# Performance work log

Hardware: AMD Instinct MI355X
Metric: run time of the kernel (lower is better)

## Reference

```python
import jax, jax.numpy as jnp
import numpy as np

N_NODES = 50000
N_EDGES = 800000
IN_FEATS, N_HIDDEN, OUT_FEATS = 512, 512, 256


def setup_inputs() -> dict:
    key = jax.random.key(0)
    ks = jax.random.split(key, 10)
    features = jax.random.normal(ks[0], (N_NODES, IN_FEATS), dtype=jnp.float32)
    src = jax.random.randint(ks[1], (N_EDGES,), 0, N_NODES, dtype=jnp.int64)
    dst = jax.random.randint(ks[2], (N_EDGES,), 0, N_NODES, dtype=jnp.int64)
    def glorot(k, fan_in, fan_out):
        s = jnp.sqrt(6.0 / (fan_in + fan_out)).astype(jnp.float32)
        return jax.random.uniform(k, (fan_in, fan_out), jnp.float32, -s, s)
    W0 = glorot(ks[3], IN_FEATS, N_HIDDEN)
    b0 = jnp.zeros((N_HIDDEN,), jnp.float32)
    W1 = glorot(ks[4], N_HIDDEN, N_HIDDEN)
    b1 = jnp.zeros((N_HIDDEN,), jnp.float32)
    W2 = glorot(ks[5], N_HIDDEN, OUT_FEATS)
    b2 = jnp.zeros((OUT_FEATS,), jnp.float32)
    return {"features": features, "src": src, "dst": dst,
            "W0": W0, "b0": b0, "W1": W1, "b1": b1, "W2": W2, "b2": b2}


def _graph_conv(x, W, b, src, dst, out_norm, in_norm, activation):
    # DGL GraphConv, norm='both': D_out^{-1/2} A^T D_in^{-1/2}? -> per-node scale,
    # gather on src, segment-sum on dst, scale, linear, bias, activation.
    h = x @ W                               # [N, out] dense GEMM (weight applied first)
    h = h * out_norm[:, None]               # src-side degree norm
    msgs = h[src]                           # [E, out] gather
    agg = jax.ops.segment_sum(msgs, dst, num_segments=x.shape[0])  # [N, out]
    agg = agg * in_norm[:, None] + b
    return activation(agg) if activation is not None else agg


def reference(features, src, dst, W0, b0, W1, b1, W2, b2):
    n = features.shape[0]
    ones = jnp.ones((src.shape[0],), jnp.float32)
    out_deg = jnp.clip(jax.ops.segment_sum(ones, src, num_segments=n), 1.0)
    in_deg = jnp.clip(jax.ops.segment_sum(ones, dst, num_segments=n), 1.0)
    out_norm = jax.lax.rsqrt(out_deg)
    in_norm = jax.lax.rsqrt(in_deg)
    # eval mode: dropout between layers is identity
    h = _graph_conv(features, W0, b0, src, dst, out_norm, in_norm, jax.nn.relu)
    h = _graph_conv(h, W1, b1, src, dst, out_norm, in_norm, jax.nn.relu)
    h = _graph_conv(h, W2, b2, src, dst, out_norm, in_norm, None)
    return h
```

## Files before the change

kernel.cpp:

```cpp
#include <hip/hip_runtime.h>

#define N_NODES 50000
#define N_EDGES 800000

typedef __attribute__((ext_vector_type(8))) _Float16 half8;
typedef __attribute__((ext_vector_type(4))) float f32x4;
typedef __attribute__((ext_vector_type(8))) unsigned short ushort8;

static __device__ __forceinline__ unsigned short f2h(float f) {
    _Float16 h = (_Float16)f;
    return __builtin_bit_cast(unsigned short, h);
}
static __device__ __forceinline__ float h2f(unsigned short u) {
    return (float)__builtin_bit_cast(_Float16, u);
}

static __device__ __forceinline__ void async16(unsigned short* lds, const unsigned short* g) {
    __builtin_amdgcn_global_load_lds(
        (const __attribute__((address_space(1))) void*)g,
        (__attribute__((address_space(3))) void*)lds, 16, 0, 0);
}

__global__ void hist_kernel(const int* __restrict__ src, const int* __restrict__ dst,
                            int* __restrict__ outc, int* __restrict__ inc) {
    int i = blockIdx.x * blockDim.x + threadIdx.x;
    if (i < N_EDGES) {
        atomicAdd(&outc[src[i]], 1);
        atomicAdd(&inc[dst[i]], 1);
    }
}

__global__ void norm_kernel(const int* __restrict__ outc, const int* __restrict__ inc,
                            float* __restrict__ outn, float* __restrict__ inn) {
    int i = blockIdx.x * blockDim.x + threadIdx.x;
    if (i < N_NODES) {
        outn[i] = rsqrtf(fmaxf((float)outc[i], 1.0f));
        inn[i]  = rsqrtf(fmaxf((float)inc[i], 1.0f));
    }
}

__global__ __launch_bounds__(256) void scan1(const int* __restrict__ cnt,
                                             int* __restrict__ row_start,
                                             int* __restrict__ bsum, int n) {
    __shared__ int t[256];
    int tid = threadIdx.x;
    int i = blockIdx.x * 256 + tid;
    int v = (i < n) ? cnt[i] : 0;
    t[tid] = v;
    __syncthreads();
#pragma unroll
    for (int off = 1; off < 256; off <<= 1) {
        int x = (tid >= off) ? t[tid - off] : 0;
        __syncthreads();
        t[tid] += x;
        __syncthreads();
    }
    if (i < n) row_start[i] = t[tid] - v;
    if (tid == 255) bsum[blockIdx.x] = t[255];
}

__global__ __launch_bounds__(256) void scan2(int* __restrict__ bsum,
                                             int* __restrict__ boff,
                                             int* __restrict__ row_start, int nb) {
    __shared__ int t[256];
    int tid = threadIdx.x;
    int v = (tid < nb) ? bsum[tid] : 0;
    t[tid] = v;
    __syncthreads();
#pragma unroll
    for (int off = 1; off < 256; off <<= 1) {
        int x = (tid >= off) ? t[tid - off] : 0;
        __syncthreads();
        t[tid] += x;
        __syncthreads();
    }
    if (tid < nb) boff[tid] = t[tid] - v;
    if (tid == 0) row_start[N_NODES] = N_EDGES;
}

__global__ __launch_bounds__(256) void scan3(int* __restrict__ row_start,
                                             const int* __restrict__ boff, int n) {
    int i = blockIdx.x * 256 + threadIdx.x;
    if (i < n) row_start[i] += boff[blockIdx.x];
}

__global__ void fill_kernel(const int* __restrict__ src, const int* __restrict__ dst,
                            const int* __restrict__ row_start, int* __restrict__ cursor,
                            int* __restrict__ csr_src) {
    int e = blockIdx.x * blockDim.x + threadIdx.x;
    if (e < N_EDGES) {
        int d = dst[e];
        int pos = atomicAdd(&cursor[d], 1);
        csr_src[row_start[d] + pos] = src[e];
    }
}

__global__ __launch_bounds__(256) void conv_W(const float* __restrict__ W,
                                              unsigned short* __restrict__ Wt,
                                              int K, int N) {
    __shared__ float t[32][33];
    int tx = threadIdx.x & 31, ty = threadIdx.x >> 5;
    int kb = blockIdx.x * 32, nb = blockIdx.y * 32;
#pragma unroll
    for (int i = 0; i < 4; ++i)
        t[ty + 8 * i][tx] = W[(size_t)(kb + ty + 8 * i) * N + nb + tx];
    __syncthreads();
#pragma unroll
    for (int i = 0; i < 4; ++i) {
        float v = t[tx][ty + 8 * i];
        int n = nb + ty + 8 * i, k = kb + tx;
        Wt[(size_t)n * K + k] = f2h(v);
    }
}

__global__ void conv_A(const float4* __restrict__ feat4, const float* __restrict__ outn,
                       ushort4* __restrict__ Af, long total4) {
    long i = (long)blockIdx.x * blockDim.x + threadIdx.x;
    if (i >= total4) return;
    int row = (int)(i >> 7);
    float s = outn[row];
    float4 v = feat4[i];
    ushort4 h;
    h.x = f2h(v.x * s);
    h.y = f2h(v.y * s);
    h.z = f2h(v.z * s);
    h.w = f2h(v.w * s);
    Af[i] = h;
}

__global__ __launch_bounds__(256) void gemm_mfma(
    const unsigned short* __restrict__ A, const unsigned short* __restrict__ B,
    unsigned short* __restrict__ C, int M, int N)
{
    const int K = 512;
    __shared__ unsigned short sA[128 * 32];
    __shared__ unsigned short sB[128 * 32];

    const int tid = threadIdx.x;
    const int rowBase = blockIdx.x * 128;
    const int colBase = blockIdx.y * 128;
    const int wave = tid >> 6;
    const int lane = tid & 63;
    const int wr = (wave >> 1) * 64;
    const int wc = (wave & 1) * 64;
    const int lrow = lane & 15;
    const int quad = lane >> 4;

    f32x4 acc[4][4] = {};

    const int crow = tid >> 2;
    const int ck   = (tid & 3) * 8;
    const int ar0 = min(rowBase + crow, M - 1);
    const int ar1 = min(rowBase + 64 + crow, M - 1);
    const int bn0 = colBase + crow;
    const int bn1 = colBase + 64 + crow;
    const int ldsOf0 = tid * 8;
    const int ldsOf1 = 64 * 32 + tid * 8;

    for (int k0 = 0; k0 < K; k0 += 32) {
        __syncthreads();
        async16(sA + ldsOf0, A + (size_t)ar0 * K + k0 + ck);
        async16(sA + ldsOf1, A + (size_t)ar1 * K + k0 + ck);
        async16(sB + ldsOf0, B + (size_t)bn0 * K + k0 + ck);
        async16(sB + ldsOf1, B + (size_t)bn1 * K + k0 + ck);
        __syncthreads();

        half8 av[4], bv[4];
#pragma unroll
        for (int mt = 0; mt < 4; ++mt)
            av[mt] = *(const half8*)&sA[(wr + mt * 16 + lrow) * 32 + quad * 8];
#pragma unroll
        for (int nt = 0; nt < 4; ++nt)
            bv[nt] = *(const half8*)&sB[(wc + nt * 16 + lrow) * 32 + quad * 8];
#pragma unroll
        for (int mt = 0; mt < 4; ++mt)
#pragma unroll
            for (int nt = 0; nt < 4; ++nt)
                acc[mt][nt] = __builtin_amdgcn_mfma_f32_16x16x32_f16(av[mt], bv[nt], acc[mt][nt], 0, 0, 0);
    }

#pragma unroll
    for (int mt = 0; mt < 4; ++mt) {
        int grow0 = rowBase + wr + mt * 16 + quad * 4;
#pragma unroll
        for (int nt = 0; nt < 4; ++nt) {
            int gcol = colBase + wc + nt * 16 + lrow;
#pragma unroll
            for (int r = 0; r < 4; ++r) {
                int grow = grow0 + r;
                if (grow < M) C[(size_t)grow * N + gcol] = f2h(acc[mt][nt][r]);
            }
        }
    }
}

__global__ __launch_bounds__(64) void agg_f16_512(
    const unsigned short* __restrict__ H, const int* __restrict__ csr_src,
    const int* __restrict__ row_start, const float* __restrict__ inn,
    const float* __restrict__ outn, const float* __restrict__ bias,
    ushort8* __restrict__ Af)
{
    const int d = blockIdx.x;
    const int tid = threadIdx.x;
    const int start = row_start[d];
    const int end   = row_start[d + 1];
    const unsigned short* Hb = H + tid * 8;

    float acc[8] = {};
    int j = start;
    for (; j + 4 <= end; j += 4) {
        int i0 = csr_src[j + 0], i1 = csr_src[j + 1];
        int i2 = csr_src[j + 2], i3 = csr_src[j + 3];
        ushort8 u0 = *(const ushort8*)(Hb + (size_t)i0 * 512);
        ushort8 u1 = *(const ushort8*)(Hb + (size_t)i1 * 512);
        ushort8 u2 = *(const ushort8*)(Hb + (size_t)i2 * 512);
        ushort8 u3 = *(const ushort8*)(Hb + (size_t)i3 * 512);
#pragma unroll
        for (int q = 0; q < 8; ++q) {
            acc[q] += h2f(u0[q]);
            acc[q] += h2f(u1[q]);
            acc[q] += h2f(u2[q]);
            acc[q] += h2f(u3[q]);
        }
    }
    for (; j < end; ++j) {
        int i0 = csr_src[j];
        ushort8 u0 = *(const ushort8*)(Hb + (size_t)i0 * 512);
#pragma unroll
        for (int q = 0; q < 8; ++q) acc[q] += h2f(u0[q]);
    }

    float s = inn[d];
    float so = outn[d];
    float b[8];
    *(float4*)&b[0] = ((const float4*)bias)[tid * 2 + 0];
    *(float4*)&b[4] = ((const float4*)bias)[tid * 2 + 1];
    ushort8 h;
#pragma unroll
    for (int q = 0; q < 8; ++q)
        h[q] = f2h(fmaxf(acc[q] * s + b[q], 0.f) * so);
    Af[(size_t)d * 64 + tid] = h;
}

__global__ __launch_bounds__(64) void agg_f32_256(
    const unsigned short* __restrict__ H, const int* __restrict__ csr_src,
    const int* __restrict__ row_start, const float* __restrict__ inn,
    const float* __restrict__ bias, float4* __restrict__ out)
{
    const int d = blockIdx.x;
    const int tid = threadIdx.x;
    const int start = row_start[d];
    const int end   = row_start[d + 1];
    const unsigned short* Hb = H + tid * 4;

    float acc[4] = {};
    int j = start;
    for (; j + 4 <= end; j += 4) {
        int i0 = csr_src[j + 0], i1 = csr_src[j + 1];
        int i2 = csr_src[j + 2], i3 = csr_src[j + 3];
        ushort4 u0 = *(const ushort4*)(Hb + (size_t)i0 * 256);
        ushort4 u1 = *(const ushort4*)(Hb + (size_t)i1 * 256);
        ushort4 u2 = *(const ushort4*)(Hb + (size_t)i2 * 256);
        ushort4 u3 = *(const ushort4*)(Hb + (size_t)i3 * 256);
        acc[0] += h2f(u0.x) + h2f(u1.x) + h2f(u2.x) + h2f(u3.x);
        acc[1] += h2f(u0.y) + h2f(u1.y) + h2f(u2.y) + h2f(u3.y);
        acc[2] += h2f(u0.z) + h2f(u1.z) + h2f(u2.z) + h2f(u3.z);
        acc[3] += h2f(u0.w) + h2f(u1.w) + h2f(u2.w) + h2f(u3.w);
    }
    for (; j < end; ++j) {
        ushort4 u0 = *(const ushort4*)(Hb + (size_t)csr_src[j] * 256);
        acc[0] += h2f(u0.x); acc[1] += h2f(u0.y);
        acc[2] += h2f(u0.z); acc[3] += h2f(u0.w);
    }

    float s = inn[d];
    float4 b = ((const float4*)bias)[tid];
    float4 r;
    r.x = acc[0] * s + b.x;
    r.y = acc[1] * s + b.y;
    r.z = acc[2] * s + b.z;
    r.w = acc[3] * s + b.w;
    out[(size_t)d * 64 + tid] = r;
}

extern "C" void kernel_launch(void* const* d_in, const int* in_sizes, int n_in,
                              void* d_out, int out_size, void* d_ws, size_t ws_size,
                              hipStream_t stream) {
    const float* feat = (const float*)d_in[0];
    const int*   src  = (const int*)d_in[1];
    const int*   dst  = (const int*)d_in[2];
    const float* W0   = (const float*)d_in[3];
    const float* b0   = (const float*)d_in[4];
    const float* W1   = (const float*)d_in[5];
    const float* b1   = (const float*)d_in[6];
    const float* W2   = (const float*)d_in[7];
    const float* b2   = (const float*)d_in[8];
    float* out = (float*)d_out;

    char* p = (char*)d_ws;
    auto alloc = [&](size_t bytes) {
        char* r = p;
        p += (bytes + 63) & ~(size_t)63;
        return r;
    };
    float* outn = (float*)alloc(N_NODES * 4);
    float* inn  = (float*)alloc(N_NODES * 4);
    int* outc      = (int*)alloc(N_NODES * 4);
    int* inc       = (int*)alloc(N_NODES * 4);
    int* cursor    = (int*)alloc(N_NODES * 4);
    int* row_start = (int*)alloc((N_NODES + 1) * 4);
    int* bsum      = (int*)alloc(256 * 4);
    int* boff      = (int*)alloc(256 * 4);
    int* csr_src   = (int*)alloc(N_EDGES * 4);
    unsigned short* W0t = (unsigned short*)alloc(512 * 512 * 2);
    unsigned short* W1t = (unsigned short*)alloc(512 * 512 * 2);
    unsigned short* W2t = (unsigned short*)alloc(256 * 512 * 2);
    unsigned short* Af  = (unsigned short*)alloc((size_t)N_NODES * 512 * 2);
    unsigned short* H   = (unsigned short*)alloc((size_t)N_NODES * 512 * 2);

    const int NB = (N_NODES + 255) / 256;

    hipMemsetAsync(outc, 0, 3 * N_NODES * sizeof(int), stream);
    hist_kernel<<<(N_EDGES + 255) / 256, 256, 0, stream>>>(src, dst, outc, inc);
    norm_kernel<<<(N_NODES + 255) / 256, 256, 0, stream>>>(outc, inc, outn, inn);
    scan1<<<NB, 256, 0, stream>>>(inc, row_start, bsum, N_NODES);
    scan2<<<1, 256, 0, stream>>>(bsum, boff, row_start, NB);
    scan3<<<NB, 256, 0, stream>>>(row_start, boff, N_NODES);
    fill_kernel<<<(N_EDGES + 255) / 256, 256, 0, stream>>>(src, dst, row_start, cursor, csr_src);

    conv_W<<<dim3(16, 16), 256, 0, stream>>>(W0, W0t, 512, 512);
    conv_W<<<dim3(16, 16), 256, 0, stream>>>(W1, W1t, 512, 512);
    conv_W<<<dim3(16, 8),  256, 0, stream>>>(W2, W2t, 512, 256);

    long total4 = (long)N_NODES * 128;
    conv_A<<<(int)((total4 + 255) / 256), 256, 0, stream>>>(
        (const float4*)feat, outn, (ushort4*)Af, total4);

    dim3 g512((N_NODES + 127) / 128, 4);
    dim3 g256((N_NODES + 127) / 128, 2);

    gemm_mfma<<<g512, 256, 0, stream>>>(Af, W0t, H, N_NODES, 512);
    agg_f16_512<<<N_NODES, 64, 0, stream>>>(
        H, csr_src, row_start, inn, outn, b0, (ushort8*)Af);

    gemm_mfma<<<g512, 256, 0, stream>>>(Af, W1t, H, N_NODES, 512);
    agg_f16_512<<<N_NODES, 64, 0, stream>>>(
        H, csr_src, row_start, inn, outn, b1, (ushort8*)Af);

    gemm_mfma<<<g256, 256, 0, stream>>>(Af, W2t, H, N_NODES, 256);
    agg_f32_256<<<N_NODES, 64, 0, stream>>>(
        H, csr_src, row_start, inn, b2, (float4*)out);
}
```

Measured before the change: 759.1 us.

## Store GEMM output in 32-column chunks and aggregate per chunk for cache locality

The GEMM epilogue now writes H in a column-chunked layout (32 fp16 columns per chunk, all nodes contiguous), so each chunk is about 3.2MB and can stay resident in cache during the gather. The aggregation kernels are rewritten so each block handles one chunk for 16 nodes. Each wave splits its edges across 4 lane groups and reduces them with shuffles. This trades wide 1KB row gathers for many small 64-byte gathers that hit a cache-resident working set. The cost is that csr_src and row_start are re-read once per chunk, and each load is only 4 bytes per lane.

```diff
diff --git a/kernel.cpp b/kernel.cpp
--- a/kernel.cpp
+++ b/kernel.cpp
@@ -5,6 +5,7 @@
 
 typedef __attribute__((ext_vector_type(8))) _Float16 half8;
 typedef __attribute__((ext_vector_type(4))) float f32x4;
+typedef __attribute__((ext_vector_type(2))) float f32x2;
 typedef __attribute__((ext_vector_type(8))) unsigned short ushort8;
 
 static __device__ __forceinline__ unsigned short f2h(float f) {
@@ -185,102 +186,113 @@
 #pragma unroll
         for (int nt = 0; nt < 4; ++nt) {
             int gcol = colBase + wc + nt * 16 + lrow;
+            size_t chunkBase = (size_t)(gcol >> 5) * M * 32 + (gcol & 31);
 #pragma unroll
             for (int r = 0; r < 4; ++r) {
                 int grow = grow0 + r;
-                if (grow < M) C[(size_t)grow * N + gcol] = f2h(acc[mt][nt][r]);
-            }
-        }
-    }
-}
-
-__global__ __launch_bounds__(64) void agg_f16_512(
+                if (grow < M) C[chunkBase + (size_t)grow * 32] = f2h(acc[mt][nt][r]);
+            }
+        }
+    }
+}
+
+__global__ __launch_bounds__(256) void agg_f16_chunked(
     const unsigned short* __restrict__ H, const int* __restrict__ csr_src,
     const int* __restrict__ row_start, const float* __restrict__ inn,
     const float* __restrict__ outn, const float* __restrict__ bias,
-    ushort8* __restrict__ Af)
+    unsigned short* __restrict__ Af)
 {
-    const int d = blockIdx.x;
-    const int tid = threadIdx.x;
-    const int start = row_start[d];
-    const int end   = row_start[d + 1];
-    const unsigned short* Hb = H + tid * 8;
-
-    float acc[8] = {};
-    int j = start;
-    for (; j + 4 <= end; j += 4) {
-        int i0 = csr_src[j + 0], i1 = csr_src[j + 1];
-        int i2 = csr_src[j + 2], i3 = csr_src[j + 3];
-        ushort8 u0 = *(const ushort8*)(Hb + (size_t)i0 * 512);
-        ushort8 u1 = *(const ushort8*)(Hb + (size_t)i1 * 512);
-        ushort8 u2 = *(const ushort8*)(Hb + (size_t)i2 * 512);
-        ushort8 u3 = *(const ushort8*)(Hb + (size_t)i3 * 512);
-#pragma unroll
-        for (int q = 0; q < 8; ++q) {
-            acc[q] += h2f(u0[q]);
-            acc[q] += h2f(u1[q]);
-            acc[q] += h2f(u2[q]);
-            acc[q] += h2f(u3[q]);
-        }
-    }
-    for (; j < end; ++j) {
-        int i0 = csr_src[j];
-        ushort8 u0 = *(const ushort8*)(Hb + (size_t)i0 * 512);
-#pragma unroll
-        for (int q = 0; q < 8; ++q) acc[q] += h2f(u0[q]);
-    }
-
-    float s = inn[d];
-    float so = outn[d];
-    float b[8];
-    *(float4*)&b[0] = ((const float4*)bias)[tid * 2 + 0];
-    *(float4*)&b[4] = ((const float4*)bias)[tid * 2 + 1];
-    ushort8 h;
-#pragma unroll
-    for (int q = 0; q < 8; ++q)
-        h[q] = f2h(fmaxf(acc[q] * s + b[q], 0.f) * so);
-    Af[(size_t)d * 64 + tid] = h;
-}
-
-__global__ __launch_bounds__(64) void agg_f32_256(
+    const int wave = threadIdx.x >> 6;
+    const int lane = threadIdx.x & 63;
+    const int g = lane >> 4;
+    const int f = lane & 15;
+    const int c = blockIdx.z * 8 + blockIdx.x;
+    const int baseNode = blockIdx.y * 16 + wave * 4;
+
+    const unsigned short* Hc = H + (size_t)c * N_NODES * 32 + 2 * f;
+    const float2 bf = ((const float2*)(bias + c * 32))[f];
+
+    for (int nn = 0; nn < 4; ++nn) {
+        int d = baseNode + nn;
+        if (d >= N_NODES) return;
+        int start = row_start[d];
+        int end   = row_start[d + 1];
+        float a0 = 0.f, a1 = 0.f;
+        for (int j = start; j < end; j += 8) {
+            int e0 = j + g, e1 = j + 4 + g;
+            if (e0 < end) {
+                int i0 = __builtin_nontemporal_load(csr_src + e0);
+                unsigned int u = *(const unsigned int*)(Hc + (size_t)i0 * 32);
+                a0 += h2f((unsigned short)(u & 0xffffu));
+                a1 += h2f((unsigned short)(u >> 16));
+            }
+            if (e1 < end) {
+                int i1 = __builtin_nontemporal_load(csr_src + e1);
+                unsigned int u = *(const unsigned int*)(Hc + (size_t)i1 * 32);
+                a0 += h2f((unsigned short)(u & 0xffffu));
+                a1 += h2f((unsigned short)(u >> 16));
+            }
+        }
+        a0 += __shfl_xor(a0, 16); a0 += __shfl_xor(a0, 32);
+        a1 += __shfl_xor(a1, 16); a1 += __shfl_xor(a1, 32);
+        if (g == 0) {
+            float s = inn[d], so = outn[d];
+            unsigned int h0 = f2h(fmaxf(a0 * s + bf.x, 0.f) * so);
+            unsigned int h1 = f2h(fmaxf(a1 * s + bf.y, 0.f) * so);
+            unsigned int pk = h0 | (h1 << 16);
+            __builtin_nontemporal_store(pk,
+                (unsigned int*)(Af + (size_t)d * 512 + c * 32) + f);
+        }
+    }
+}
+
+__global__ __launch_bounds__(256) void agg_f32_chunked(
     const unsigned short* __restrict__ H, const int* __restrict__ csr_src,
     const int* __restrict__ row_start, const float* __restrict__ inn,
-    const float* __restrict__ bias, float4* __restrict__ out)
+    const float* __restrict__ bias, float* __restrict__ out)
 {
-    const int d = blockIdx.x;
-    const int tid = threadIdx.x;
-    const int start = row_start[d];
-    const int end   = row_start[d + 1];
-    const unsigned short* Hb = H + tid * 4;
-
-    float acc[4] = {};
-    int j = start;
-    for (; j + 4 <= end; j += 4) {
-        int i0 = csr_src[j + 0], i1 = csr_src[j + 1];
-        int i2 = csr_src[j + 2], i3 = csr_src[j + 3];
-        ushort4 u0 = *(const ushort4*)(Hb + (size_t)i0 * 256);
-        ushort4 u1 = *(const ushort4*)(Hb + (size_t)i1 * 256);
-        ushort4 u2 = *(const ushort4*)(Hb + (size_t)i2 * 256);
-        ushort4 u3 = *(const ushort4*)(Hb + (size_t)i3 * 256);
-        acc[0] += h2f(u0.x) + h2f(u1.x) + h2f(u2.x) + h2f(u3.x);
-        acc[1] += h2f(u0.y) + h2f(u1.y) + h2f(u2.y) + h2f(u3.y);
-        acc[2] += h2f(u0.z) + h2f(u1.z) + h2f(u2.z) + h2f(u3.z);
-        acc[3] += h2f(u0.w) + h2f(u1.w) + h2f(u2.w) + h2f(u3.w);
-    }
-    for (; j < end; ++j) {
-        ushort4 u0 = *(const ushort4*)(Hb + (size_t)csr_src[j] * 256);
-        acc[0] += h2f(u0.x); acc[1] += h2f(u0.y);
-        acc[2] += h2f(u0.z); acc[3] += h2f(u0.w);
-    }
-
-    float s = inn[d];
-    float4 b = ((const float4*)bias)[tid];
-    float4 r;
-    r.x = acc[0] * s + b.x;
-    r.y = acc[1] * s + b.y;
-    r.z = acc[2] * s + b.z;
-    r.w = acc[3] * s + b.w;
-    out[(size_t)d * 64 + tid] = r;
+    const int wave = threadIdx.x >> 6;
+    const int lane = threadIdx.x & 63;
+    const int g = lane >> 4;
+    const int f = lane & 15;
+    const int c = blockIdx.x;
+    const int baseNode = blockIdx.y * 16 + wave * 4;
+
+    const unsigned short* Hc = H + (size_t)c * N_NODES * 32 + 2 * f;
+    const float2 bf = ((const float2*)(bias + c * 32))[f];
+
+    for (int nn = 0; nn < 4; ++nn) {
+        int d = baseNode + nn;
+        if (d >= N_NODES) return;
+        int start = row_start[d];
+        int end   = row_start[d + 1];
+        float a0 = 0.f, a1 = 0.f;
+        for (int j = start; j < end; j += 8) {
+            int e0 = j + g, e1 = j + 4 + g;
+            if (e0 < end) {
+                int i0 = __builtin_nontemporal_load(csr_src + e0);
+                unsigned int u = *(const unsigned int*)(Hc + (size_t)i0 * 32);
+                a0 += h2f((unsigned short)(u & 0xffffu));
+                a1 += h2f((unsigned short)(u >> 16));
+            }
+            if (e1 < end) {
+                int i1 = __builtin_nontemporal_load(csr_src + e1);
+                unsigned int u = *(const unsigned int*)(Hc + (size_t)i1 * 32);
+                a0 += h2f((unsigned short)(u & 0xffffu));
+                a1 += h2f((unsigned short)(u >> 16));
+            }
+        }
+        a0 += __shfl_xor(a0, 16); a0 += __shfl_xor(a0, 32);
+        a1 += __shfl_xor(a1, 16); a1 += __shfl_xor(a1, 32);
+        if (g == 0) {
+            float s = inn[d];
+            f32x2 r;
+            r.x = a0 * s + bf.x;
+            r.y = a1 * s + bf.y;
+            __builtin_nontemporal_store(r,
+                (f32x2*)(out + (size_t)d * 256 + c * 32) + f);
+        }
+    }
 }
 
 extern "C" void kernel_launch(void* const* d_in, const int* in_sizes, int n_in,
@@ -338,16 +350,19 @@
 
     dim3 g512((N_NODES + 127) / 128, 4);
     dim3 g256((N_NODES + 127) / 128, 2);
+    const int NT = (N_NODES + 15) / 16;
+    dim3 gAgg512(8, NT, 2);
+    dim3 gAgg256(8, NT, 1);
 
     gemm_mfma<<<g512, 256, 0, stream>>>(Af, W0t, H, N_NODES, 512);
-    agg_f16_512<<<N_NODES, 64, 0, stream>>>(
-        H, csr_src, row_start, inn, outn, b0, (ushort8*)Af);
+    agg_f16_chunked<<<gAgg512, 256, 0, stream>>>(
+        H, csr_src, row_start, inn, outn, b0, Af);
 
     gemm_mfma<<<g512, 256, 0, stream>>>(Af, W1t, H, N_NODES, 512);
-    agg_f16_512<<<N_NODES, 64, 0, stream>>>(
-        H, csr_src, row_start, inn, outn, b1, (ushort8*)Af);
+    agg_f16_chunked<<<gAgg512, 256, 0, stream>>>(
+        H, csr_src, row_start, inn, outn, b1, Af);
 
     gemm_mfma<<<g256, 256, 0, stream>>>(Af, W2t, H, N_NODES, 256);
-    agg_f32_256<<<N_NODES, 64, 0, stream>>>(
-        H, csr_src, row_start, inn, b2, (float4*)out);
-}
+    agg_f32_chunked<<<gAgg256, 256, 0, stream>>>(
+        H, csr_src, row_start, inn, b2, out);
+}
```

Measured after the change: 1.471 ms. 93.8% more time.

## Degree-sort nodes and gather from column-chunked GEMM output for aggregation

Applied to the files above, without the earlier changes.

The GEMM now writes its output in 32-column chunks laid out node-major within each chunk, so each chunk of H is a compact 64-byte-per-node array. Aggregation kernels are rewritten so each block covers one feature chunk for 64 nodes, and nodes are ordered by in-degree through a bucket sort so that nodes within a wavefront have similar degrees. Neighbor indices are staged in LDS, and the gathers are meant to hit the L2 cache better because each chunk's working set is small. This adds three preprocessing kernels, and the output writes are now scattered by degree order rather than sequential.

```diff
diff --git a/kernel.cpp b/kernel.cpp
--- a/kernel.cpp
+++ b/kernel.cpp
@@ -5,6 +5,7 @@
 
 typedef __attribute__((ext_vector_type(8))) _Float16 half8;
 typedef __attribute__((ext_vector_type(4))) float f32x4;
+typedef __attribute__((ext_vector_type(4))) int i32x4;
 typedef __attribute__((ext_vector_type(8))) unsigned short ushort8;
 
 static __device__ __forceinline__ unsigned short f2h(float f) {
@@ -92,6 +93,40 @@
         int d = dst[e];
         int pos = atomicAdd(&cursor[d], 1);
         csr_src[row_start[d] + pos] = src[e];
+    }
+}
+
+__global__ void bucket_hist(const int* __restrict__ inc, int* __restrict__ bcnt) {
+    int i = blockIdx.x * blockDim.x + threadIdx.x;
+    if (i < N_NODES) atomicAdd(&bcnt[min(inc[i], 1023)], 1);
+}
+
+__global__ __launch_bounds__(1024) void bucket_scan(const int* __restrict__ bcnt,
+                                                    int* __restrict__ boff2) {
+    __shared__ int t[1024];
+    int tid = threadIdx.x;
+    int v = bcnt[tid];
+    t[tid] = v;
+    __syncthreads();
+#pragma unroll
+    for (int off = 1; off < 1024; off <<= 1) {
+        int x = (tid >= off) ? t[tid - off] : 0;
+        __syncthreads();
+        t[tid] += x;
+        __syncthreads();
+    }
+    boff2[tid] = t[tid] - v;
+}
+
+__global__ void bucket_scatter(const int* __restrict__ inc, const int* __restrict__ row_start,
+                               int* __restrict__ bcur, i32x4* __restrict__ pmeta) {
+    int i = blockIdx.x * blockDim.x + threadIdx.x;
+    if (i < N_NODES) {
+        int deg = inc[i];
+        int p = atomicAdd(&bcur[min(deg, 1023)], 1);
+        i32x4 m;
+        m.x = i; m.y = row_start[i]; m.z = deg; m.w = 0;
+        pmeta[p] = m;
     }
 }
 
@@ -185,102 +220,133 @@
 #pragma unroll
         for (int nt = 0; nt < 4; ++nt) {
             int gcol = colBase + wc + nt * 16 + lrow;
+            size_t chunkBase = (size_t)(gcol >> 5) * M * 32 + (gcol & 31);
 #pragma unroll
             for (int r = 0; r < 4; ++r) {
                 int grow = grow0 + r;
-                if (grow < M) C[(size_t)grow * N + gcol] = f2h(acc[mt][nt][r]);
+                if (grow < M) C[chunkBase + (size_t)grow * 32] = f2h(acc[mt][nt][r]);
             }
         }
     }
 }
 
-__global__ __launch_bounds__(64) void agg_f16_512(
+#define KB 64
+
+__global__ __launch_bounds__(256) void agg_f16_v3(
     const unsigned short* __restrict__ H, const int* __restrict__ csr_src,
-    const int* __restrict__ row_start, const float* __restrict__ inn,
+    const i32x4* __restrict__ pmeta, const float* __restrict__ inn,
     const float* __restrict__ outn, const float* __restrict__ bias,
-    ushort8* __restrict__ Af)
+    unsigned short* __restrict__ Af)
 {
-    const int d = blockIdx.x;
-    const int tid = threadIdx.x;
-    const int start = row_start[d];
-    const int end   = row_start[d + 1];
-    const unsigned short* Hb = H + tid * 8;
-
-    float acc[8] = {};
-    int j = start;
-    for (; j + 4 <= end; j += 4) {
-        int i0 = csr_src[j + 0], i1 = csr_src[j + 1];
-        int i2 = csr_src[j + 2], i3 = csr_src[j + 3];
-        ushort8 u0 = *(const ushort8*)(Hb + (size_t)i0 * 512);
-        ushort8 u1 = *(const ushort8*)(Hb + (size_t)i1 * 512);
-        ushort8 u2 = *(const ushort8*)(Hb + (size_t)i2 * 512);
-        ushort8 u3 = *(const ushort8*)(Hb + (size_t)i3 * 512);
-#pragma unroll
-        for (int q = 0; q < 8; ++q) {
-            acc[q] += h2f(u0[q]);
-            acc[q] += h2f(u1[q]);
-            acc[q] += h2f(u2[q]);
-            acc[q] += h2f(u3[q]);
+    __shared__ int sIdx[4][16][68];
+    const int tid = threadIdx.x, lane = tid & 63, w = tid >> 6;
+    const int s = lane >> 2, f = lane & 3;
+    const int c = blockIdx.z * 8 + blockIdx.x;
+    const int t = blockIdx.y * 64 + w * 16 + s;
+
+    int d = 0, st = 0, deg = 0;
+    if (t < N_NODES) {
+        i32x4 m = __builtin_nontemporal_load(pmeta + t);
+        d = m.x; st = m.y; deg = m.z;
+    }
+    int wmax = deg;
+    wmax = max(wmax, __shfl_xor(wmax, 4));
+    wmax = max(wmax, __shfl_xor(wmax, 8));
+    wmax = max(wmax, __shfl_xor(wmax, 16));
+    wmax = max(wmax, __shfl_xor(wmax, 32));
+
+    const unsigned short* Hc = H + (size_t)c * (N_NODES * 32);
+    int* slab = &sIdx[w][s][0];
+    float a[8] = {};
+
+    for (int kb = 0; kb < wmax; kb += KB) {
+        const int kend = min(deg - kb, KB);
+        const int klim = min(wmax - kb, KB);
+        for (int i = f; i < kend; i += 4)
+            slab[i] = __builtin_nontemporal_load(csr_src + st + kb + i);
+        asm volatile("s_waitcnt lgkmcnt(0)" ::: "memory");
+        for (int k = 0; k < klim; ++k) {
+            int idx = slab[k];
+            if (k < kend) {
+                const ushort8 u = *(const ushort8*)(Hc + (unsigned)idx * 32u + (unsigned)f * 8u);
+#pragma unroll
+                for (int q = 0; q < 8; ++q) a[q] += h2f(u[q]);
+            }
         }
-    }
-    for (; j < end; ++j) {
-        int i0 = csr_src[j];
-        ushort8 u0 = *(const ushort8*)(Hb + (size_t)i0 * 512);
-#pragma unroll
-        for (int q = 0; q < 8; ++q) acc[q] += h2f(u0[q]);
-    }
-
-    float s = inn[d];
-    float so = outn[d];
-    float b[8];
-    *(float4*)&b[0] = ((const float4*)bias)[tid * 2 + 0];
-    *(float4*)&b[4] = ((const float4*)bias)[tid * 2 + 1];
-    ushort8 h;
-#pragma unroll
-    for (int q = 0; q < 8; ++q)
-        h[q] = f2h(fmaxf(acc[q] * s + b[q], 0.f) * so);
-    Af[(size_t)d * 64 + tid] = h;
-}
-
-__global__ __launch_bounds__(64) void agg_f32_256(
+        asm volatile("" ::: "memory");
+    }
+
+    if (t < N_NODES) {
+        float si = inn[d], so = outn[d];
+        float b8[8];
+        *(float4*)&b8[0] = *(const float4*)(bias + c * 32 + f * 8);
+        *(float4*)&b8[4] = *(const float4*)(bias + c * 32 + f * 8 + 4);
+        ushort8 h;
+#pragma unroll
+        for (int q = 0; q < 8; ++q)
+            h[q] = f2h(fmaxf(a[q] * si + b8[q], 0.f) * so);
+        __builtin_nontemporal_store(h,
+            (ushort8*)(Af + (size_t)d * 512 + c * 32 + f * 8));
+    }
+}
+
+__global__ __launch_bounds__(256) void agg_f32_v3(
     const unsigned short* __restrict__ H, const int* __restrict__ csr_src,
-    const int* __restrict__ row_start, const float* __restrict__ inn,
-    const float* __restrict__ bias, float4* __restrict__ out)
+    const i32x4* __restrict__ pmeta, const float* __restrict__ inn,
+    const float* __restrict__ bias, float* __restrict__ out)
 {
-    const int d = blockIdx.x;
-    const int tid = threadIdx.x;
-    const int start = row_start[d];
-    const int end   = row_start[d + 1];
-    const unsigned short* Hb = H + tid * 4;
-
-    float acc[4] = {};
-    int j = start;
-    for (; j + 4 <= end; j += 4) {
-        int i0 = csr_src[j + 0], i1 = csr_src[j + 1];
-        int i2 = csr_src[j + 2], i3 = csr_src[j + 3];
-        ushort4 u0 = *(const ushort4*)(Hb + (size_t)i0 * 256);
-        ushort4 u1 = *(const ushort4*)(Hb + (size_t)i1 * 256);
-        ushort4 u2 = *(const ushort4*)(Hb + (size_t)i2 * 256);
-        ushort4 u3 = *(const ushort4*)(Hb + (size_t)i3 * 256);
-        acc[0] += h2f(u0.x) + h2f(u1.x) + h2f(u2.x) + h2f(u3.x);
-        acc[1] += h2f(u0.y) + h2f(u1.y) + h2f(u2.y) + h2f(u3.y);
-        acc[2] += h2f(u0.z) + h2f(u1.z) + h2f(u2.z) + h2f(u3.z);
-        acc[3] += h2f(u0.w) + h2f(u1.w) + h2f(u2.w) + h2f(u3.w);
-    }
-    for (; j < end; ++j) {
-        ushort4 u0 = *(const ushort4*)(Hb + (size_t)csr_src[j] * 256);
-        acc[0] += h2f(u0.x); acc[1] += h2f(u0.y);
-        acc[2] += h2f(u0.z); acc[3] += h2f(u0.w);
-    }
-
-    float s = inn[d];
-    float4 b = ((const float4*)bias)[tid];
-    float4 r;
-    r.x = acc[0] * s + b.x;
-    r.y = acc[1] * s + b.y;
-    r.z = acc[2] * s + b.z;
-    r.w = acc[3] * s + b.w;
-    out[(size_t)d * 64 + tid] = r;
+    __shared__ int sIdx[4][16][68];
+    const int tid = threadIdx.x, lane = tid & 63, w = tid >> 6;
+    const int s = lane >> 2, f = lane & 3;
+    const int c = blockIdx.x;
+    const int t = blockIdx.y * 64 + w * 16 + s;
+
+    int d = 0, st = 0, deg = 0;
+    if (t < N_NODES) {
+        i32x4 m = __builtin_nontemporal_load(pmeta + t);
+        d = m.x; st = m.y; deg = m.z;
+    }
+    int wmax = deg;
+    wmax = max(wmax, __shfl_xor(wmax, 4));
+    wmax = max(wmax, __shfl_xor(wmax, 8));
+    wmax = max(wmax, __shfl_xor(wmax, 16));
+    wmax = max(wmax, __shfl_xor(wmax, 32));
+
+    const unsigned short* Hc = H + (size_t)c * (N_NODES * 32);
+    int* slab = &sIdx[w][s][0];
+    float a[8] = {};
+
+    for (int kb = 0; kb < wmax; kb += KB) {
+        const int kend = min(deg - kb, KB);
+        const int klim = min(wmax - kb, KB);
+        for (int i = f; i < kend; i += 4)
+            slab[i] = __builtin_nontemporal_load(csr_src + st + kb + i);
+        asm volatile("s_waitcnt lgkmcnt(0)" ::: "memory");
+        for (int k = 0; k < klim; ++k) {
+            int idx = slab[k];
+            if (k < kend) {
+                const ushort8 u = *(const ushort8*)(Hc + (unsigned)idx * 32u + (unsigned)f * 8u);
+#pragma unroll
+                for (int q = 0; q < 8; ++q) a[q] += h2f(u[q]);
+            }
+        }
+        asm volatile("" ::: "memory");
+    }
+
+    if (t < N_NODES) {
+        float si = inn[d];
+        float b8[8];
+        *(float4*)&b8[0] = *(const float4*)(bias + c * 32 + f * 8);
+        *(float4*)&b8[4] = *(const float4*)(bias + c * 32 + f * 8 + 4);
+        f32x4 r0, r1;
+        r0.x = a[0] * si + b8[0]; r0.y = a[1] * si + b8[1];
+        r0.z = a[2] * si + b8[2]; r0.w = a[3] * si + b8[3];
+        r1.x = a[4] * si + b8[4]; r1.y = a[5] * si + b8[5];
+        r1.z = a[6] * si + b8[6]; r1.w = a[7] * si + b8[7];
+        float* op = out + (size_t)d * 256 + c * 32 + f * 8;
+        __builtin_nontemporal_store(r0, (f32x4*)op);
+        __builtin_nontemporal_store(r1, (f32x4*)(op + 4));
+    }
 }
 
 extern "C" void kernel_launch(void* const* d_in, const int* in_sizes, int n_in,
@@ -308,10 +374,13 @@
     int* outc      = (int*)alloc(N_NODES * 4);
     int* inc       = (int*)alloc(N_NODES * 4);
     int* cursor    = (int*)alloc(N_NODES * 4);
+    int* bcnt      = (int*)alloc(1024 * 4);
     int* row_start = (int*)alloc((N_NODES + 1) * 4);
     int* bsum      = (int*)alloc(256 * 4);
     int* boff      = (int*)alloc(256 * 4);
+    int* boff2     = (int*)alloc(1024 * 4);
     int* csr_src   = (int*)alloc(N_EDGES * 4);
+    i32x4* pmeta   = (i32x4*)alloc((size_t)(N_NODES + 64) * 16);
     unsigned short* W0t = (unsigned short*)alloc(512 * 512 * 2);
     unsigned short* W1t = (unsigned short*)alloc(512 * 512 * 2);
     unsigned short* W2t = (unsigned short*)alloc(256 * 512 * 2);
@@ -320,13 +389,16 @@
 
     const int NB = (N_NODES + 255) / 256;
 
-    hipMemsetAsync(outc, 0, 3 * N_NODES * sizeof(int), stream);
+    hipMemsetAsync(outc, 0, (size_t)3 * N_NODES * 4 + 1024 * 4, stream);
     hist_kernel<<<(N_EDGES + 255) / 256, 256, 0, stream>>>(src, dst, outc, inc);
     norm_kernel<<<(N_NODES + 255) / 256, 256, 0, stream>>>(outc, inc, outn, inn);
     scan1<<<NB, 256, 0, stream>>>(inc, row_start, bsum, N_NODES);
     scan2<<<1, 256, 0, stream>>>(bsum, boff, row_start, NB);
     scan3<<<NB, 256, 0, stream>>>(row_start, boff, N_NODES);
     fill_kernel<<<(N_EDGES + 255) / 256, 256, 0, stream>>>(src, dst, row_start, cursor, csr_src);
+    bucket_hist<<<NB, 256, 0, stream>>>(inc, bcnt);
+    bucket_scan<<<1, 1024, 0, stream>>>(bcnt, boff2);
+    bucket_scatter<<<NB, 256, 0, stream>>>(inc, row_start, boff2, pmeta);
 
     conv_W<<<dim3(16, 16), 256, 0, stream>>>(W0, W0t, 512, 512);
     conv_W<<<dim3(16, 16), 256, 0, stream>>>(W1, W1t, 512, 512);
@@ -338,16 +410,19 @@
 
     dim3 g512((N_NODES + 127) / 128, 4);
     dim3 g256((N_NODES + 127) / 128, 2);
+    const int NTB = (N_NODES + 63) / 64;
+    dim3 gAgg512(8, NTB, 2);
+    dim3 gAgg256(8, NTB, 1);
 
     gemm_mfma<<<g512, 256, 0, stream>>>(Af, W0t, H, N_NODES, 512);
-    agg_f16_512<<<N_NODES, 64, 0, stream>>>(
-        H, csr_src, row_start, inn, outn, b0, (ushort8*)Af);
+    agg_f16_v3<<<gAgg512, 256, 0, stream>>>(
+        H, csr_src, pmeta, inn, outn, b0, Af);
 
     gemm_mfma<<<g512, 256, 0, stream>>>(Af, W1t, H, N_NODES, 512);
-    agg_f16_512<<<N_NODES, 64, 0, stream>>>(
-        H, csr_src, row_start, inn, outn, b1, (ushort8*)Af);
+    agg_f16_v3<<<gAgg512, 256, 0, stream>>>(
+        H, csr_src, pmeta, inn, outn, b1, Af);
 
     gemm_mfma<<<g256, 256, 0, stream>>>(Af, W2t, H, N_NODES, 256);
-    agg_f32_256<<<N_NODES, 64, 0, stream>>>(
-        H, csr_src, row_start, inn, b2, (float4*)out);
-}
+    agg_f32_v3<<<gAgg256, 256, 0, stream>>>(
+        H, csr_src, pmeta, inn, b2, out);
+}
```

Result: slower. 1.066 ms (+40.4%).
